# Kernel optimization log

Hardware: AMD Instinct MI355X
Metric: run time of the kernel (lower is better)

The kernel has to match this reference:

```python
import jax, jax.numpy as jnp
import numpy as np

B, N, C, H, W = 16, 8, 3, 64, 96
PRED_BITS = 2
CONV_CH, FC, FMAP_H, FMAP_W = 16, 100, 16, 24


def _conv(x, Wc, bc):
    # x: [n, cin, 64, 96] -> [n, 16, 16, 24]; kernel 8x8, stride 4, pad 2
    y = jax.lax.conv_general_dilated(x, Wc, (4, 4), [(2, 2), (2, 2)],
                                     dimension_numbers=('NCHW', 'OIHW', 'NCHW'))
    return y + bc[None, :, None, None]


def _encoder(x, Wc, bc, W2, b2, W3, b3):
    h1 = jax.nn.relu(_conv(x, Wc, bc)).reshape(x.shape[0], -1)  # [n, 6144]
    h2 = jax.nn.relu(h1 @ W2 + b2)
    return h2 @ W3 + b3  # [n, PRED_BITS]


def _gumbel_softmax(logits, g, temp):
    return jax.nn.softmax((logits + g) / temp, axis=-1)


def setup_inputs() -> dict:
    key = jax.random.key(0)
    ks = jax.random.split(key, 16)
    rn = lambda k, s, sc=1.0: jax.random.normal(k, s, jnp.float32) * sc
    gum = lambda k, s: -jnp.log(-jnp.log(jax.random.uniform(k, s, jnp.float32, 1e-6, 1.0 - 1e-6)))
    inp = {
        'state': rn(ks[0], (B, N, C, H, W)),
        'state_next': rn(ks[1], (B, N, C, H, W)),
        'state_tilda': rn(ks[2], (B, N, C, H, W)),
        'n_obj': jax.random.randint(ks[3], (B,), 1, N + 1),
        'temp': jnp.asarray(1.0, jnp.float32),
        'g_unary': gum(ks[4], (3, B * N, PRED_BITS)),
        'g_binary': gum(ks[5], (3, B * N * N, PRED_BITS)),
        'Wc_u': rn(ks[6], (CONV_CH, C, 8, 8), 0.05),
        'bc_u': jnp.zeros((CONV_CH,), jnp.float32),
        'W2_u': rn(ks[7], (CONV_CH * FMAP_H * FMAP_W, FC), 0.02),
        'b2_u': jnp.zeros((FC,), jnp.float32),
        'W3_u': rn(ks[8], (FC, PRED_BITS), 0.1),
        'b3_u': jnp.zeros((PRED_BITS,), jnp.float32),
        'Wc_b': rn(ks[9], (CONV_CH, 2 * C, 8, 8), 0.05),
        'bc_b': jnp.zeros((CONV_CH,), jnp.float32),
        'W2_b': rn(ks[10], (CONV_CH * FMAP_H * FMAP_W, FC), 0.02),
        'b2_b': jnp.zeros((FC,), jnp.float32),
        'W3_b': rn(ks[11], (FC, PRED_BITS), 0.1),
        'b3_b': jnp.zeros((PRED_BITS,), jnp.float32),
    }
    return inp


def reference(state, state_next, state_tilda, n_obj, temp, g_unary, g_binary,
              Wc_u, bc_u, W2_u, b2_u, W3_u, b3_u,
              Wc_b, bc_b, W2_b, b2_b, W3_b, b3_b):
    # cartesian-product pair gather (padded to N_max^2 per sample)
    ii = jnp.arange(N * N) // N
    jj = jnp.arange(N * N) % N

    def pairs(s):  # [B,N,C,H,W] -> [B*N*N, 2C, H, W]
        return jnp.concatenate([s[:, ii], s[:, jj]], axis=2).reshape(B * N * N, 2 * C, H, W)

    def bin_pred(s, g):
        logits = _encoder(pairs(s), Wc_b, bc_b, W2_b, b2_b, W3_b, b3_b)
        return _gumbel_softmax(logits, g, temp).reshape(B, N * N, PRED_BITS)

    def un_pred(s, g):
        logits = _encoder(s.reshape(B * N, C, H, W), Wc_u, bc_u, W2_u, b2_u, W3_u, b3_u)
        return _gumbel_softmax(logits, g, temp).reshape(B, N, PRED_BITS)

    bp = bin_pred(state, g_binary[0])
    bp_n = bin_pred(state_next, g_binary[1])
    bp_t = bin_pred(state_tilda, g_binary[2])
    up = un_pred(state, g_unary[0])
    up_n = un_pred(state_next, g_unary[1])
    up_t = un_pred(state_tilda, g_unary[2])

    # compact the valid n^2 pairs to the front (matches torch padded scatter layout)
    n = n_obj[:, None]                      # [B,1]
    p = jnp.arange(N * N)[None, :]          # [1,N^2]
    ns = jnp.maximum(n, 1)
    k = (p // ns) * N + (p % ns)            # padded index of compact position p
    valid_b = (p < n * n)[:, :, None]
    kidx = jnp.clip(k, 0, N * N - 1)[:, :, None]

    def compact(x):
        return jnp.take_along_axis(x, kidx, axis=1) * valid_b

    valid_u = (jnp.arange(N)[None, :] < n)[:, :, None]

    return (compact(bp), compact(bp_n), compact(bp_t),
            up * valid_u, up_n * valid_u, up_t * valid_u)
```

## Files before the change

kernel.cpp:

```cpp
#include <hip/hip_runtime.h>
#include <hip/hip_bf16.h>


typedef __attribute__((ext_vector_type(8))) short bf16x8;
typedef __attribute__((ext_vector_type(4))) float f32x4;

__device__ inline unsigned short bf16u(float x) {
    __hip_bfloat16 h = __float2bfloat16(x);
    return __builtin_bit_cast(unsigned short, h);
}

__global__ __launch_bounds__(256) void convertB_kernel(
    const float* __restrict__ W2b, const float* __restrict__ W2u,
    const float* __restrict__ Wcu, const float* __restrict__ Wcb,
    unsigned short* __restrict__ Btb, unsigned short* __restrict__ Btu,
    unsigned short* __restrict__ BwFrag)
{
    const int bx = blockIdx.x;
    const int tid = threadIdx.x;
    if (bx == 96) {
        for (int t = tid; t < 18 * 64; t += 256) {
            int lane = t & 63, g = t >> 6;
            int t6 = g / 3, nt = g % 3;
            int ch = lane & 15, kq = lane >> 4;
            unsigned short* dst = BwFrag + (long)t * 8;
#pragma unroll
            for (int j = 0; j < 8; ++j) {
                int e = t6 * 32 + kq * 8 + j;
                float v = (nt == 0) ? Wcu[ch * 192 + e]
                        : (nt == 1) ? Wcb[ch * 384 + e]
                                    : Wcb[ch * 384 + 192 + e];
                dst[j] = bf16u(v);
            }
        }
        return;
    }
    const int arr = bx / 48;
    const int k0 = (bx % 48) * 128;
    const float* W2 = arr ? W2u : W2b;
    unsigned short* Bt = arr ? Btu : Btb;
    __shared__ unsigned short lds[128 * 130];
    for (int t = tid; t < 128 * 128; t += 256) {
        int kk = t >> 7, f = t & 127;
        float v = (f < 100) ? W2[(long)(k0 + kk) * 100 + f] : 0.f;
        lds[kk * 130 + f] = bf16u(v);
    }
    __syncthreads();
    for (int t = tid; t < 128 * 128; t += 256) {
        int f = t >> 7, kk = t & 127;
        Bt[(long)f * 6144 + k0 + kk] = lds[kk * 130 + f];
    }
}

#define CL_STRIDE 106
#define CL_CH (36 * CL_STRIDE)
__global__ __launch_bounds__(256) void convmfma_kernel(
    const float* __restrict__ s0, const float* __restrict__ s1, const float* __restrict__ s2,
    const unsigned short* __restrict__ BwFrag,
    const float* __restrict__ bcu, const float* __restrict__ bcb,
    unsigned short* __restrict__ A, float* __restrict__ yf, float* __restrict__ ys)
{
    const int bx  = blockIdx.x;
    const int si  = bx >> 8;
    const int rem = bx & 255;
    const int img = rem >> 1;
    const int h   = rem & 1;
    const float* simg = (si == 0 ? s0 : (si == 1 ? s1 : s2)) + (long)img * 18432;

    __shared__ __align__(16) unsigned short ldsimg[3 * CL_CH];
    const int tid  = threadIdx.x;
    const int lane = tid & 63;
    const int w    = tid >> 6;
    const int quad = lane >> 4;
    const int lcol = lane & 15;

    bf16x8 bw[6][3];
#pragma unroll
    for (int t6 = 0; t6 < 6; ++t6)
#pragma unroll
        for (int nt = 0; nt < 3; ++nt)
            bw[t6][nt] = *(const bf16x8*)(BwFrag + ((t6 * 3 + nt) * 64 + lane) * 8);

    for (int t = tid; t < (3 * CL_CH) / 2; t += 256)
        ((unsigned*)ldsimg)[t] = 0u;
    __syncthreads();

    const int y0 = h * 32;
    for (int t = tid; t < 3 * 36 * 24; t += 256) {
        int c = t / 864, rq = t % 864, r = rq / 24, q = rq % 24;
        int iy = y0 + r - 2;
        if (iy >= 0 && iy < 64) {
            float4 v = *((const float4*)(simg + c * 6144 + iy * 96) + q);
            unsigned lo = (unsigned)bf16u(v.x) | ((unsigned)bf16u(v.y) << 16);
            unsigned hi = (unsigned)bf16u(v.z) | ((unsigned)bf16u(v.w) << 16);
            unsigned* dst = (unsigned*)(ldsimg + c * CL_CH + r * CL_STRIDE + q * 4 + 4);
            dst[0] = lo; dst[1] = hi;
        }
    }
    __syncthreads();

    const float bu = bcu[lcol];
    const float bb = bcb[lcol];
    const long im = (long)si * 128 + img;
    unsigned short* Arow = A + (3072 + im) * 6144;
    float* yfr = yf + im * 6144;
    float* ysr = ys + im * 6144;

#pragma unroll
    for (int mi = 0; mi < 3; ++mi) {
        const int mt = w * 3 + mi;
        const int p  = mt * 16 + lcol;
        const int oyl = p / 24, ox = p % 24;
        f32x4 a0 = {0.f, 0.f, 0.f, 0.f}, a1 = a0, a2 = a0;
#pragma unroll
        for (int t6 = 0; t6 < 6; ++t6) {
            int g  = t6 * 4 + quad;
            int c  = g >> 3, ky = g & 7;
            const unsigned* lp = (const unsigned*)(ldsimg + c * CL_CH + (oyl * 4 + ky) * CL_STRIDE + ox * 4 + 2);
            bf16x8 afr;
            unsigned* ap = (unsigned*)&afr;
            ap[0] = lp[0]; ap[1] = lp[1]; ap[2] = lp[2]; ap[3] = lp[3];
            a0 = __builtin_amdgcn_mfma_f32_16x16x32_bf16(afr, bw[t6][0], a0, 0, 0, 0);
            a1 = __builtin_amdgcn_mfma_f32_16x16x32_bf16(afr, bw[t6][1], a1, 0, 0, 0);
            a2 = __builtin_amdgcn_mfma_f32_16x16x32_bf16(afr, bw[t6][2], a2, 0, 0, 0);
        }
#pragma unroll
        for (int reg = 0; reg < 4; ++reg) {
            int pr = h * 192 + mt * 16 + quad * 4 + reg;
            float u = a0[reg] + bu;
            Arow[lcol * 384 + pr] = bf16u(u > 0.f ? u : 0.f);
            yfr[lcol * 384 + pr] = a1[reg] + bb;
            ysr[lcol * 384 + pr] = a2[reg];
        }
    }
}

__global__ __launch_bounds__(256) void expand_kernel(
    const float* __restrict__ yf, const float* __restrict__ ys, unsigned short* __restrict__ A)
{
    const int bx  = blockIdx.x;
    const int si  = bx >> 7;
    const int rem = bx & 127;
    const int b   = rem >> 3;
    const int tid = threadIdx.x;
    const float* fr = yf + (long)bx * 6144;
    const long rowbase = ((long)si * 1024 + (long)b * 64 + (long)(rem & 7) * 8) * 6144;

    for (int chunk = 0; chunk < 6; ++chunk) {
        int k = chunk * 1024 + tid * 4;
        float4 vf = *(const float4*)(fr + k);
#pragma unroll
        for (int j = 0; j < 8; ++j) {
            float4 vs = *(const float4*)(ys + ((long)si * 128 + b * 8 + j) * 6144 + k);
            float x0 = vf.x + vs.x, x1 = vf.y + vs.y, x2 = vf.z + vs.z, x3 = vf.w + vs.w;
            ushort4 o;
            o.x = bf16u(x0 > 0.f ? x0 : 0.f);
            o.y = bf16u(x1 > 0.f ? x1 : 0.f);
            o.z = bf16u(x2 > 0.f ? x2 : 0.f);
            o.w = bf16u(x3 > 0.f ? x3 : 0.f);
            *(ushort4*)(A + rowbase + (long)j * 6144 + k) = o;
        }
    }
}

__global__ __launch_bounds__(256) void gemm_kernel(
    const unsigned short* __restrict__ A,
    const unsigned short* __restrict__ Btb, const unsigned short* __restrict__ Btu,
    float* __restrict__ partial)
{
    const int tid = threadIdx.x;
    const int mt = blockIdx.x % 27;
    const int kc = blockIdx.x / 27;
    const unsigned short* Bt = (mt < 24) ? Btb : Btu;

    __shared__ __align__(16) unsigned short lsA[128 * 72];
    __shared__ __align__(16) unsigned short lsB[128 * 72];

    const int lane = tid & 63;
    const int w  = tid >> 6;
    const int wr = w & 1;
    const int wc = w >> 1;
    const int quad = lane >> 4;
    const int lcol = lane & 15;

    f32x4 acc[4][4];
#pragma unroll
    for (int i = 0; i < 4; ++i)
#pragma unroll
        for (int j = 0; j < 4; ++j) acc[i][j] = (f32x4){0.f, 0.f, 0.f, 0.f};

    const int r = tid >> 1;
    const int h = tid & 1;
    const long arow = (long)(mt * 128 + r) * 6144;
    const long brow = (long)r * 6144;
    const int kbase0 = kc * 768;

    for (int it = 0; it < 12; ++it) {
        const int kb = kbase0 + it * 64;
        const unsigned short* ga = A + arow + kb + h * 32;
        const unsigned short* gb = Bt + brow + kb + h * 32;
        unsigned short* da = lsA + r * 72 + h * 32;
        unsigned short* db = lsB + r * 72 + h * 32;
#pragma unroll
        for (int i = 0; i < 4; ++i) {
            *(uint4*)(da + i * 8) = *(const uint4*)(ga + i * 8);
            *(uint4*)(db + i * 8) = *(const uint4*)(gb + i * 8);
        }
        __syncthreads();
#pragma unroll
        for (int ks = 0; ks < 2; ++ks) {
            bf16x8 af[4], bfr[4];
#pragma unroll
            for (int t = 0; t < 4; ++t)
                af[t] = *(const bf16x8*)(lsA + (wr * 64 + t * 16 + lcol) * 72 + ks * 32 + quad * 8);
#pragma unroll
            for (int t = 0; t < 4; ++t)
                bfr[t] = *(const bf16x8*)(lsB + (wc * 64 + t * 16 + lcol) * 72 + ks * 32 + quad * 8);
#pragma unroll
            for (int i = 0; i < 4; ++i)
#pragma unroll
                for (int j = 0; j < 4; ++j)
                    acc[i][j] = __builtin_amdgcn_mfma_f32_16x16x32_bf16(af[i], bfr[j], acc[i][j], 0, 0, 0);
        }
        __syncthreads();
    }

    float* out = partial + (long)(kc * 27 + mt) * 16384;
#pragma unroll
    for (int i = 0; i < 4; ++i)
#pragma unroll
        for (int j = 0; j < 4; ++j)
#pragma unroll
            for (int reg = 0; reg < 4; ++reg) {
                int rr = wr * 64 + i * 16 + quad * 4 + reg;
                int cc = wc * 64 + j * 16 + lcol;
                out[rr * 128 + cc] = acc[i][j][reg];
            }
}

__global__ __launch_bounds__(256) void reduce_kernel(
    const float* __restrict__ partial,
    const float* __restrict__ b2b, const float* __restrict__ b2u,
    float* __restrict__ h2)
{
    int gid = blockIdx.x * 256 + threadIdx.x;
    if (gid >= 3456 * 112) return;
    int m = gid / 112, f = gid % 112;
    int mt = m >> 7, rr = m & 127;
    float s = 0.f;
#pragma unroll
    for (int kc = 0; kc < 8; ++kc)
        s += partial[((long)(kc * 27 + mt) * 128 + rr) * 128 + f];
    float v = 0.f;
    if (f < 100) {
        s += (m < 3072) ? b2b[f] : b2u[f];
        v = s > 0.f ? s : 0.f;
    }
    h2[(long)m * 112 + f] = v;
}

__device__ inline void fc2_dot(const float* __restrict__ hr, const float* __restrict__ W3,
                               float& l0, float& l1)
{
#pragma unroll 5
    for (int f4 = 0; f4 < 25; ++f4) {
        float4 hv = *(const float4*)(hr + f4 * 4);
        float4 w0 = *(const float4*)(W3 + f4 * 8);
        float4 w1 = *(const float4*)(W3 + f4 * 8 + 4);
        l0 = fmaf(hv.x, w0.x, fmaf(hv.y, w0.z, fmaf(hv.z, w1.x, fmaf(hv.w, w1.z, l0))));
        l1 = fmaf(hv.x, w0.y, fmaf(hv.y, w0.w, fmaf(hv.z, w1.y, fmaf(hv.w, w1.w, l1))));
    }
}

__global__ __launch_bounds__(64) void head_kernel(
    const float* __restrict__ h2,
    const float* __restrict__ W3b, const float* __restrict__ b3b,
    const float* __restrict__ W3u, const float* __restrict__ b3u,
    const float* __restrict__ gb, const float* __restrict__ gu,
    const int* __restrict__ nobj, const float* __restrict__ temp_p,
    float* __restrict__ out)
{
    int gid = blockIdx.x * 64 + threadIdx.x;
    if (gid >= 3456) return;
    float temp = temp_p[0];
    if (gid < 3072) {
        int si = gid / 1024, rem = gid % 1024;
        int b = rem >> 6, p = rem & 63;
        int n = nobj[b];
        int ns = n > 0 ? n : 1;
        int k = (p / ns) * 8 + (p % ns);
        int valid = p < n * n;
        int kk = k < 63 ? k : 63;
        const float* hr = h2 + (long)(si * 1024 + b * 64 + kk) * 112;
        float l0 = b3b[0], l1 = b3b[1];
        fc2_dot(hr, W3b, l0, l1);
        const float* g = gb + (long)(si * 1024 + b * 64 + kk) * 2;
        float d = ((l0 + g[0]) - (l1 + g[1])) / temp;
        float p0 = 1.f / (1.f + expf(-d));
        float* o = out + (long)si * 2048 + (b * 64 + p) * 2;
        o[0] = valid ? p0 : 0.f;
        o[1] = valid ? 1.f - p0 : 0.f;
    } else {
        int r = gid - 3072;
        int si = r / 128, q = r % 128;
        int b = q >> 3, i = q & 7;
        const float* hr = h2 + (long)(3072 + r) * 112;
        float l0 = b3u[0], l1 = b3u[1];
        fc2_dot(hr, W3u, l0, l1);
        const float* g = gu + (long)si * 256 + (b * 8 + i) * 2;
        float d = ((l0 + g[0]) - (l1 + g[1])) / temp;
        float p0 = 1.f / (1.f + expf(-d));
        int valid = i < nobj[b];
        float* o = out + 6144 + (long)si * 256 + (b * 8 + i) * 2;
        o[0] = valid ? p0 : 0.f;
        o[1] = valid ? 1.f - p0 : 0.f;
    }
}

static const size_t A_OFF    = 0;
static const size_t YF_OFF   = 42467328;
static const size_t YS_OFF   = 51904512;
static const size_t BTB_OFF  = 61341696;
static const size_t BTU_OFF  = 62914560;
static const size_t PART_OFF = 64487424;
static const size_t H2_OFF   = 78643200;
static const size_t BWF_OFF  = 80191488;

extern "C" void kernel_launch(void* const* d_in, const int* in_sizes, int n_in,
                              void* d_out, int out_size, void* d_ws, size_t ws_size,
                              hipStream_t stream) {
    const float* state   = (const float*)d_in[0];
    const float* state_n = (const float*)d_in[1];
    const float* state_t = (const float*)d_in[2];
    const int*   n_obj   = (const int*)  d_in[3];
    const float* temp    = (const float*)d_in[4];
    const float* g_un    = (const float*)d_in[5];
    const float* g_bin   = (const float*)d_in[6];
    const float* Wc_u    = (const float*)d_in[7];
    const float* bc_u    = (const float*)d_in[8];
    const float* W2_u    = (const float*)d_in[9];
    const float* b2_u    = (const float*)d_in[10];
    const float* W3_u    = (const float*)d_in[11];
    const float* b3_u    = (const float*)d_in[12];
    const float* Wc_b    = (const float*)d_in[13];
    const float* bc_b    = (const float*)d_in[14];
    const float* W2_b    = (const float*)d_in[15];
    const float* b2_b    = (const float*)d_in[16];
    const float* W3_b    = (const float*)d_in[17];
    const float* b3_b    = (const float*)d_in[18];

    char* ws = (char*)d_ws;
    unsigned short* A    = (unsigned short*)(ws + A_OFF);
    float*          yf   = (float*)(ws + YF_OFF);
    float*          ys   = (float*)(ws + YS_OFF);
    unsigned short* Btb  = (unsigned short*)(ws + BTB_OFF);
    unsigned short* Btu  = (unsigned short*)(ws + BTU_OFF);
    float*          prt  = (float*)(ws + PART_OFF);
    float*          h2   = (float*)(ws + H2_OFF);
    unsigned short* BwF  = (unsigned short*)(ws + BWF_OFF);
    float*          out  = (float*)d_out;

    hipLaunchKernelGGL(convertB_kernel, dim3(97), dim3(256), 0, stream,
                       W2_b, W2_u, Wc_u, Wc_b, Btb, Btu, BwF);
    hipLaunchKernelGGL(convmfma_kernel, dim3(768), dim3(256), 0, stream,
                       state, state_n, state_t, BwF, bc_u, bc_b, A, yf, ys);
    hipLaunchKernelGGL(expand_kernel, dim3(384), dim3(256), 0, stream,
                       yf, ys, A);
    hipLaunchKernelGGL(gemm_kernel, dim3(216), dim3(256), 0, stream,
                       A, Btb, Btu, prt);
    hipLaunchKernelGGL(reduce_kernel, dim3(1512), dim3(256), 0, stream,
                       prt, b2_b, b2_u, h2);
    hipLaunchKernelGGL(head_kernel, dim3(54), dim3(64), 0, stream,
                       h2, W3_b, b3_b, W3_u, b3_u, g_bin, g_un, n_obj, temp, out);
}
```

Measured before the change: 182.0 us.

## Fuse pair expansion into GEMM A-load and merge reduce with FC2 head

Removes the expand kernel that materialised the full 3072x6144 bf16 pair activation matrix. The GEMM now builds each pair row on the fly while loading A, summing the bf16 first-image and second-image conv features and applying ReLU. The conv intermediates are stored as bf16 rather than fp32, and the conv epilogue writes them with vector stores. The GEMM M tile shrinks to 64 rows with double the block count, and the partial-sum reduce is fused with the FC2 dot product using shuffles. Storing the pre-sum features in bf16 adds a little rounding before the sum, and the smaller tiles reduce reuse of B.

```diff
diff --git a/kernel.cpp b/kernel.cpp
--- a/kernel.cpp
+++ b/kernel.cpp
@@ -8,6 +8,14 @@
 __device__ inline unsigned short bf16u(float x) {
     __hip_bfloat16 h = __float2bfloat16(x);
     return __builtin_bit_cast(unsigned short, h);
+}
+
+__device__ inline unsigned pair_relu(unsigned f, unsigned s) {
+    float lo = __builtin_bit_cast(float, f << 16) + __builtin_bit_cast(float, s << 16);
+    float hi = __builtin_bit_cast(float, f & 0xffff0000u) + __builtin_bit_cast(float, s & 0xffff0000u);
+    lo = lo > 0.f ? lo : 0.f;
+    hi = hi > 0.f ? hi : 0.f;
+    return (unsigned)bf16u(lo) | ((unsigned)bf16u(hi) << 16);
 }
 
 __global__ __launch_bounds__(256) void convertB_kernel(
@@ -58,7 +66,8 @@
     const float* __restrict__ s0, const float* __restrict__ s1, const float* __restrict__ s2,
     const unsigned short* __restrict__ BwFrag,
     const float* __restrict__ bcu, const float* __restrict__ bcb,
-    unsigned short* __restrict__ A, float* __restrict__ yf, float* __restrict__ ys)
+    unsigned short* __restrict__ Au, unsigned short* __restrict__ yfb,
+    unsigned short* __restrict__ ysb)
 {
     const int bx  = blockIdx.x;
     const int si  = bx >> 8;
@@ -102,9 +111,9 @@
     const float bu = bcu[lcol];
     const float bb = bcb[lcol];
     const long im = (long)si * 128 + img;
-    unsigned short* Arow = A + (3072 + im) * 6144;
-    float* yfr = yf + im * 6144;
-    float* ysr = ys + im * 6144;
+    unsigned short* Aur = Au + im * 6144;
+    unsigned short* yfr = yfb + im * 6144;
+    unsigned short* ysr = ysb + im * 6144;
 
 #pragma unroll
     for (int mi = 0; mi < 3; ++mi) {
@@ -124,56 +133,36 @@
             a1 = __builtin_amdgcn_mfma_f32_16x16x32_bf16(afr, bw[t6][1], a1, 0, 0, 0);
             a2 = __builtin_amdgcn_mfma_f32_16x16x32_bf16(afr, bw[t6][2], a2, 0, 0, 0);
         }
-#pragma unroll
-        for (int reg = 0; reg < 4; ++reg) {
-            int pr = h * 192 + mt * 16 + quad * 4 + reg;
-            float u = a0[reg] + bu;
-            Arow[lcol * 384 + pr] = bf16u(u > 0.f ? u : 0.f);
-            yfr[lcol * 384 + pr] = a1[reg] + bb;
-            ysr[lcol * 384 + pr] = a2[reg];
-        }
-    }
-}
-
-__global__ __launch_bounds__(256) void expand_kernel(
-    const float* __restrict__ yf, const float* __restrict__ ys, unsigned short* __restrict__ A)
-{
-    const int bx  = blockIdx.x;
-    const int si  = bx >> 7;
-    const int rem = bx & 127;
-    const int b   = rem >> 3;
-    const int tid = threadIdx.x;
-    const float* fr = yf + (long)bx * 6144;
-    const long rowbase = ((long)si * 1024 + (long)b * 64 + (long)(rem & 7) * 8) * 6144;
-
-    for (int chunk = 0; chunk < 6; ++chunk) {
-        int k = chunk * 1024 + tid * 4;
-        float4 vf = *(const float4*)(fr + k);
-#pragma unroll
-        for (int j = 0; j < 8; ++j) {
-            float4 vs = *(const float4*)(ys + ((long)si * 128 + b * 8 + j) * 6144 + k);
-            float x0 = vf.x + vs.x, x1 = vf.y + vs.y, x2 = vf.z + vs.z, x3 = vf.w + vs.w;
-            ushort4 o;
-            o.x = bf16u(x0 > 0.f ? x0 : 0.f);
-            o.y = bf16u(x1 > 0.f ? x1 : 0.f);
-            o.z = bf16u(x2 > 0.f ? x2 : 0.f);
-            o.w = bf16u(x3 > 0.f ? x3 : 0.f);
-            *(ushort4*)(A + rowbase + (long)j * 6144 + k) = o;
-        }
+        const int base = h * 192 + mt * 16 + quad * 4;
+        ushort4 ou, of, os;
+        {
+            float u0 = a0[0] + bu, u1 = a0[1] + bu, u2 = a0[2] + bu, u3 = a0[3] + bu;
+            ou.x = bf16u(u0 > 0.f ? u0 : 0.f);
+            ou.y = bf16u(u1 > 0.f ? u1 : 0.f);
+            ou.z = bf16u(u2 > 0.f ? u2 : 0.f);
+            ou.w = bf16u(u3 > 0.f ? u3 : 0.f);
+            of.x = bf16u(a1[0] + bb); of.y = bf16u(a1[1] + bb);
+            of.z = bf16u(a1[2] + bb); of.w = bf16u(a1[3] + bb);
+            os.x = bf16u(a2[0]); os.y = bf16u(a2[1]);
+            os.z = bf16u(a2[2]); os.w = bf16u(a2[3]);
+        }
+        *(ushort4*)(Aur + lcol * 384 + base) = ou;
+        *(ushort4*)(yfr + lcol * 384 + base) = of;
+        *(ushort4*)(ysr + lcol * 384 + base) = os;
     }
 }
 
 __global__ __launch_bounds__(256) void gemm_kernel(
-    const unsigned short* __restrict__ A,
+    const unsigned short* __restrict__ yfb, const unsigned short* __restrict__ ysb,
+    const unsigned short* __restrict__ Au,
     const unsigned short* __restrict__ Btb, const unsigned short* __restrict__ Btu,
     float* __restrict__ partial)
 {
     const int tid = threadIdx.x;
-    const int mt = blockIdx.x % 27;
-    const int kc = blockIdx.x / 27;
-    const unsigned short* Bt = (mt < 24) ? Btb : Btu;
-
-    __shared__ __align__(16) unsigned short lsA[128 * 72];
+    const int mt = blockIdx.x % 54;
+    const int kc = blockIdx.x / 54;
+
+    __shared__ __align__(16) unsigned short lsA[64 * 72];
     __shared__ __align__(16) unsigned short lsB[128 * 72];
 
     const int lane = tid & 63;
@@ -183,41 +172,59 @@
     const int quad = lane >> 4;
     const int lcol = lane & 15;
 
-    f32x4 acc[4][4];
-#pragma unroll
-    for (int i = 0; i < 4; ++i)
+    f32x4 acc[2][4];
+#pragma unroll
+    for (int i = 0; i < 2; ++i)
 #pragma unroll
         for (int j = 0; j < 4; ++j) acc[i][j] = (f32x4){0.f, 0.f, 0.f, 0.f};
 
-    const int r = tid >> 1;
-    const int h = tid & 1;
-    const long arow = (long)(mt * 128 + r) * 6144;
-    const long brow = (long)r * 6144;
+    const int ra = tid >> 2, qa = tid & 3;
+    const bool fused = (mt < 48);
+    const unsigned short *pf, *ps = nullptr;
+    if (fused) {
+        int g = mt * 64 + ra;
+        int si = g >> 10, gs = g & 1023;
+        int b = gs >> 6, i = (gs >> 3) & 7, j = gs & 7;
+        pf = yfb + (long)(si * 128 + b * 8 + i) * 6144;
+        ps = ysb + (long)(si * 128 + b * 8 + j) * 6144;
+    } else {
+        pf = Au + (long)((mt - 48) * 64 + ra) * 6144;
+    }
+    const unsigned short* Bt = fused ? Btb : Btu;
+    const int rb = tid >> 1, hb = tid & 1;
+    const long brow = (long)rb * 6144;
     const int kbase0 = kc * 768;
 
     for (int it = 0; it < 12; ++it) {
         const int kb = kbase0 + it * 64;
-        const unsigned short* ga = A + arow + kb + h * 32;
-        const unsigned short* gb = Bt + brow + kb + h * 32;
-        unsigned short* da = lsA + r * 72 + h * 32;
-        unsigned short* db = lsB + r * 72 + h * 32;
-#pragma unroll
-        for (int i = 0; i < 4; ++i) {
-            *(uint4*)(da + i * 8) = *(const uint4*)(ga + i * 8);
-            *(uint4*)(db + i * 8) = *(const uint4*)(gb + i * 8);
-        }
+        const uint4* gb = (const uint4*)(Bt + brow + kb + hb * 32);
+        uint4 b0 = gb[0], b1 = gb[1], b2 = gb[2], b3 = gb[3];
+        const uint4* gf = (const uint4*)(pf + kb + qa * 16);
+        uint4 f0 = gf[0], f1 = gf[1];
+        if (fused) {
+            const uint4* gs2 = (const uint4*)(ps + kb + qa * 16);
+            uint4 s0 = gs2[0], s1 = gs2[1];
+            f0.x = pair_relu(f0.x, s0.x); f0.y = pair_relu(f0.y, s0.y);
+            f0.z = pair_relu(f0.z, s0.z); f0.w = pair_relu(f0.w, s0.w);
+            f1.x = pair_relu(f1.x, s1.x); f1.y = pair_relu(f1.y, s1.y);
+            f1.z = pair_relu(f1.z, s1.z); f1.w = pair_relu(f1.w, s1.w);
+        }
+        uint4* da = (uint4*)(lsA + ra * 72 + qa * 16);
+        uint4* db = (uint4*)(lsB + rb * 72 + hb * 32);
+        da[0] = f0; da[1] = f1;
+        db[0] = b0; db[1] = b1; db[2] = b2; db[3] = b3;
         __syncthreads();
 #pragma unroll
         for (int ks = 0; ks < 2; ++ks) {
-            bf16x8 af[4], bfr[4];
-#pragma unroll
-            for (int t = 0; t < 4; ++t)
-                af[t] = *(const bf16x8*)(lsA + (wr * 64 + t * 16 + lcol) * 72 + ks * 32 + quad * 8);
+            bf16x8 af[2], bfr[4];
+#pragma unroll
+            for (int t = 0; t < 2; ++t)
+                af[t] = *(const bf16x8*)(lsA + (wr * 32 + t * 16 + lcol) * 72 + ks * 32 + quad * 8);
 #pragma unroll
             for (int t = 0; t < 4; ++t)
                 bfr[t] = *(const bf16x8*)(lsB + (wc * 64 + t * 16 + lcol) * 72 + ks * 32 + quad * 8);
 #pragma unroll
-            for (int i = 0; i < 4; ++i)
+            for (int i = 0; i < 2; ++i)
 #pragma unroll
                 for (int j = 0; j < 4; ++j)
                     acc[i][j] = __builtin_amdgcn_mfma_f32_16x16x32_bf16(af[i], bfr[j], acc[i][j], 0, 0, 0);
@@ -225,57 +232,57 @@
         __syncthreads();
     }
 
-    float* out = partial + (long)(kc * 27 + mt) * 16384;
-#pragma unroll
-    for (int i = 0; i < 4; ++i)
+    float* out = partial + (long)(kc * 54 + mt) * 8192;
+#pragma unroll
+    for (int i = 0; i < 2; ++i)
 #pragma unroll
         for (int j = 0; j < 4; ++j)
 #pragma unroll
             for (int reg = 0; reg < 4; ++reg) {
-                int rr = wr * 64 + i * 16 + quad * 4 + reg;
+                int rr = wr * 32 + i * 16 + quad * 4 + reg;
                 int cc = wc * 64 + j * 16 + lcol;
                 out[rr * 128 + cc] = acc[i][j][reg];
             }
 }
 
-__global__ __launch_bounds__(256) void reduce_kernel(
+__global__ __launch_bounds__(256) void reducefc2_kernel(
     const float* __restrict__ partial,
     const float* __restrict__ b2b, const float* __restrict__ b2u,
-    float* __restrict__ h2)
-{
-    int gid = blockIdx.x * 256 + threadIdx.x;
-    if (gid >= 3456 * 112) return;
-    int m = gid / 112, f = gid % 112;
-    int mt = m >> 7, rr = m & 127;
-    float s = 0.f;
-#pragma unroll
-    for (int kc = 0; kc < 8; ++kc)
-        s += partial[((long)(kc * 27 + mt) * 128 + rr) * 128 + f];
-    float v = 0.f;
-    if (f < 100) {
-        s += (m < 3072) ? b2b[f] : b2u[f];
-        v = s > 0.f ? s : 0.f;
-    }
-    h2[(long)m * 112 + f] = v;
-}
-
-__device__ inline void fc2_dot(const float* __restrict__ hr, const float* __restrict__ W3,
-                               float& l0, float& l1)
-{
-#pragma unroll 5
-    for (int f4 = 0; f4 < 25; ++f4) {
-        float4 hv = *(const float4*)(hr + f4 * 4);
-        float4 w0 = *(const float4*)(W3 + f4 * 8);
-        float4 w1 = *(const float4*)(W3 + f4 * 8 + 4);
-        l0 = fmaf(hv.x, w0.x, fmaf(hv.y, w0.z, fmaf(hv.z, w1.x, fmaf(hv.w, w1.z, l0))));
-        l1 = fmaf(hv.x, w0.y, fmaf(hv.y, w0.w, fmaf(hv.z, w1.y, fmaf(hv.w, w1.w, l1))));
-    }
-}
-
-__global__ __launch_bounds__(64) void head_kernel(
-    const float* __restrict__ h2,
     const float* __restrict__ W3b, const float* __restrict__ b3b,
     const float* __restrict__ W3u, const float* __restrict__ b3u,
+    float* __restrict__ logits)
+{
+    const int tid = threadIdx.x;
+    const int m = blockIdx.x * 16 + (tid >> 4);
+    const int c = tid & 15;
+    const int mt = m >> 6, rr = m & 63;
+    const bool un = (m >= 3072);
+    const float* b2 = un ? b2u : b2b;
+    const float* W3 = un ? W3u : W3b;
+    float l0 = 0.f, l1 = 0.f;
+    for (int f = c; f < 100; f += 16) {
+        float s = b2[f];
+#pragma unroll
+        for (int kc = 0; kc < 8; ++kc)
+            s += partial[((long)(kc * 54 + mt) * 64 + rr) * 128 + f];
+        float hv = s > 0.f ? s : 0.f;
+        l0 = fmaf(hv, W3[f * 2],     l0);
+        l1 = fmaf(hv, W3[f * 2 + 1], l1);
+    }
+#pragma unroll
+    for (int off = 8; off >= 1; off >>= 1) {
+        l0 += __shfl_xor(l0, off);
+        l1 += __shfl_xor(l1, off);
+    }
+    if (c == 0) {
+        const float* b3 = un ? b3u : b3b;
+        logits[m * 2]     = l0 + b3[0];
+        logits[m * 2 + 1] = l1 + b3[1];
+    }
+}
+
+__global__ __launch_bounds__(64) void final_kernel(
+    const float* __restrict__ logits,
     const float* __restrict__ gb, const float* __restrict__ gu,
     const int* __restrict__ nobj, const float* __restrict__ temp_p,
     float* __restrict__ out)
@@ -291,10 +298,9 @@
         int k = (p / ns) * 8 + (p % ns);
         int valid = p < n * n;
         int kk = k < 63 ? k : 63;
-        const float* hr = h2 + (long)(si * 1024 + b * 64 + kk) * 112;
-        float l0 = b3b[0], l1 = b3b[1];
-        fc2_dot(hr, W3b, l0, l1);
-        const float* g = gb + (long)(si * 1024 + b * 64 + kk) * 2;
+        int src = si * 1024 + b * 64 + kk;
+        float l0 = logits[src * 2], l1 = logits[src * 2 + 1];
+        const float* g = gb + (long)src * 2;
         float d = ((l0 + g[0]) - (l1 + g[1])) / temp;
         float p0 = 1.f / (1.f + expf(-d));
         float* o = out + (long)si * 2048 + (b * 64 + p) * 2;
@@ -304,27 +310,26 @@
         int r = gid - 3072;
         int si = r / 128, q = r % 128;
         int b = q >> 3, i = q & 7;
-        const float* hr = h2 + (long)(3072 + r) * 112;
-        float l0 = b3u[0], l1 = b3u[1];
-        fc2_dot(hr, W3u, l0, l1);
-        const float* g = gu + (long)si * 256 + (b * 8 + i) * 2;
+        int src = 3072 + r;
+        float l0 = logits[src * 2], l1 = logits[src * 2 + 1];
+        const float* g = gu + (long)si * 256 + q * 2;
         float d = ((l0 + g[0]) - (l1 + g[1])) / temp;
         float p0 = 1.f / (1.f + expf(-d));
         int valid = i < nobj[b];
-        float* o = out + 6144 + (long)si * 256 + (b * 8 + i) * 2;
+        float* o = out + 6144 + (long)si * 256 + q * 2;
         o[0] = valid ? p0 : 0.f;
         o[1] = valid ? 1.f - p0 : 0.f;
     }
 }
 
-static const size_t A_OFF    = 0;
-static const size_t YF_OFF   = 42467328;
-static const size_t YS_OFF   = 51904512;
-static const size_t BTB_OFF  = 61341696;
-static const size_t BTU_OFF  = 62914560;
-static const size_t PART_OFF = 64487424;
-static const size_t H2_OFF   = 78643200;
-static const size_t BWF_OFF  = 80191488;
+static const size_t YFB_OFF  = 0;
+static const size_t YSB_OFF  = 4718592;
+static const size_t AU_OFF   = 9437184;
+static const size_t BTB_OFF  = 14155776;
+static const size_t BTU_OFF  = 15728640;
+static const size_t PART_OFF = 17301504;
+static const size_t LOG_OFF  = 31457280;
+static const size_t BWF_OFF  = 31484928;
 
 extern "C" void kernel_launch(void* const* d_in, const int* in_sizes, int n_in,
                               void* d_out, int out_size, void* d_ws, size_t ws_size,
@@ -350,26 +355,24 @@
     const float* b3_b    = (const float*)d_in[18];
 
     char* ws = (char*)d_ws;
-    unsigned short* A    = (unsigned short*)(ws + A_OFF);
-    float*          yf   = (float*)(ws + YF_OFF);
-    float*          ys   = (float*)(ws + YS_OFF);
+    unsigned short* yfb  = (unsigned short*)(ws + YFB_OFF);
+    unsigned short* ysb  = (unsigned short*)(ws + YSB_OFF);
+    unsigned short* Au   = (unsigned short*)(ws + AU_OFF);
     unsigned short* Btb  = (unsigned short*)(ws + BTB_OFF);
     unsigned short* Btu  = (unsigned short*)(ws + BTU_OFF);
     float*          prt  = (float*)(ws + PART_OFF);
-    float*          h2   = (float*)(ws + H2_OFF);
+    float*          lg   = (float*)(ws + LOG_OFF);
     unsigned short* BwF  = (unsigned short*)(ws + BWF_OFF);
     float*          out  = (float*)d_out;
 
     hipLaunchKernelGGL(convertB_kernel, dim3(97), dim3(256), 0, stream,
                        W2_b, W2_u, Wc_u, Wc_b, Btb, Btu, BwF);
     hipLaunchKernelGGL(convmfma_kernel, dim3(768), dim3(256), 0, stream,
-                       state, state_n, state_t, BwF, bc_u, bc_b, A, yf, ys);
-    hipLaunchKernelGGL(expand_kernel, dim3(384), dim3(256), 0, stream,
-                       yf, ys, A);
-    hipLaunchKernelGGL(gemm_kernel, dim3(216), dim3(256), 0, stream,
-                       A, Btb, Btu, prt);
-    hipLaunchKernelGGL(reduce_kernel, dim3(1512), dim3(256), 0, stream,
-                       prt, b2_b, b2_u, h2);
-    hipLaunchKernelGGL(head_kernel, dim3(54), dim3(64), 0, stream,
-                       h2, W3_b, b3_b, W3_u, b3_u, g_bin, g_un, n_obj, temp, out);
-}
+                       state, state_n, state_t, BwF, bc_u, bc_b, Au, yfb, ysb);
+    hipLaunchKernelGGL(gemm_kernel, dim3(432), dim3(256), 0, stream,
+                       yfb, ysb, Au, Btb, Btu, prt);
+    hipLaunchKernelGGL(reducefc2_kernel, dim3(216), dim3(256), 0, stream,
+                       prt, b2_b, b2_u, W3_b, b3_b, W3_u, b3_u, lg);
+    hipLaunchKernelGGL(final_kernel, dim3(54), dim3(64), 0, stream,
+                       lg, g_bin, g_un, n_obj, temp, out);
+}
```

New measurement: 165.8 us. 1.1x faster.
